# Optimization experiments

Measured on AMD Instinct MI355X. Metric: run time of the kernel, lower is better.

## Reference

```python
import jax, jax.numpy as jnp
import numpy as np

IN_C = 1024
MID = 256
S_C = 256
TOPK_FRAC = 0.25  # atten_topk in (0,1) -> fraction of H*W


def stanh(x):
    return 1.7159 * jnp.tanh(2.0 * x / 3.0)


def setup_inputs() -> dict:
    key = jax.random.key(0)
    ks = jax.random.split(key, 5)
    B, H, W = 32, 28, 28
    x = jax.random.normal(ks[0], (B, IN_C, H, W), jnp.float32)
    s = jax.random.normal(ks[1], (B, S_C), jnp.float32)
    Wq_w = jax.random.normal(ks[2], (MID, IN_C), jnp.float32) * 0.02
    Wq_b = jnp.zeros((MID,), jnp.float32)
    Uq_w = jax.random.normal(ks[3], (MID, S_C), jnp.float32) * 0.02
    w_w = jax.random.normal(ks[4], (IN_C, MID), jnp.float32) * 0.02
    w_b = jnp.zeros((IN_C,), jnp.float32)
    return {"x": x, "s": s, "Wq_w": Wq_w, "Wq_b": Wq_b, "Uq_w": Uq_w, "w_w": w_w, "w_b": w_b}


def reference(x, s, Wq_w, Wq_b, Uq_w, w_w, w_b):
    B, C, H, W = x.shape
    # 1x1 conv Wq(x) + Uq(s) broadcast over spatial, then scaled tanh
    proj = (jnp.einsum('bchw,mc->bmhw', x, Wq_w)
            + Wq_b[None, :, None, None]
            + jnp.einsum('bs,ms->bm', s, Uq_w)[:, :, None, None])
    sig = stanh(proj)  # [B, MID, H, W]
    # 1x1 conv back to in_channel
    alpha = jnp.einsum('bmhw,cm->bchw', sig, w_w) + w_b[None, :, None, None]
    alpha = alpha.reshape(B, C, H * W)
    # topk threshold per (b, c): zero out entries strictly below the k-th largest
    k = int(TOPK_FRAC * H * W)
    th = jax.lax.top_k(alpha, k)[0][..., -1:]  # [B, C, 1]
    alpha = jnp.where(alpha < th, jnp.zeros_like(alpha), alpha)
    # softmax over spatial dim (zeros still contribute exp(0), matching torch)
    atten = jax.nn.softmax(alpha, axis=2)  # [B, C, HW]
    # weighted spatial reduce: c[b,c] = sum_n x[b,c,n] * atten[b,c,n]
    c = jnp.einsum('bcn,bcn->bc', x.reshape(B, C, -1), atten)
    return (c, atten)
```

## Files before the change

### kernel.cpp

```cpp
#include <hip/hip_runtime.h>
#include <hip/hip_bf16.h>
#include <hip/hip_fp16.h>
#include <math.h>

#define BATCH 32
#define INC 1024
#define MIDC 256
#define SC 256
#define HW 784
#define ROWS 25088
#define KSEL 196

typedef _Float16 f16;
typedef __attribute__((ext_vector_type(8))) _Float16 hfrag;
typedef __attribute__((ext_vector_type(4))) float f4;

struct alignas(8) h4s { f16 x, y, z, w; };

__device__ inline float stanh_fast(float p) {
    float e = __expf(1.33333333f * p);
    return 1.7159f * (1.0f - 2.0f / (e + 1.0f));
}

__global__ __launch_bounds__(256) void cvt_f16(const float* __restrict__ src,
                                               f16* __restrict__ dst, int n4) {
    int i = blockIdx.x * 256 + threadIdx.x;
    if (i >= n4) return;
    float4 v = ((const float4*)src)[i];
    h4s h = { (f16)v.x, (f16)v.y, (f16)v.z, (f16)v.w };
    ((h4s*)dst)[i] = h;
}

__global__ __launch_bounds__(256) void prep_x(const float* __restrict__ x,
                                              f16* __restrict__ xh) {
    int b = blockIdx.z, c0 = blockIdx.y * 32, n0 = blockIdx.x * 32;
    __shared__ float tile[32][33];
    int t = threadIdx.x;
    int r = t >> 3, cg = (t & 7) * 4;
    if (n0 + cg + 3 < HW) {
        float4 v = *(const float4*)(x + (size_t)(b * INC + c0 + r) * HW + n0 + cg);
        tile[r][cg + 0] = v.x; tile[r][cg + 1] = v.y;
        tile[r][cg + 2] = v.z; tile[r][cg + 3] = v.w;
    }
    __syncthreads();
    int rn = t >> 3, cg2 = (t & 7) * 4;
    int n = n0 + rn;
    if (n < HW) {
        h4s h = { (f16)tile[cg2 + 0][rn], (f16)tile[cg2 + 1][rn],
                  (f16)tile[cg2 + 2][rn], (f16)tile[cg2 + 3][rn] };
        *(h4s*)(xh + ((size_t)b * HW + n) * INC + c0 + cg2) = h;
    }
}

__global__ __launch_bounds__(256) void calc_u(const float* __restrict__ s,
                                              const float* __restrict__ Uq_w,
                                              const float* __restrict__ Wq_b,
                                              float* __restrict__ u) {
    __shared__ float ssh[SC];
    int b = blockIdx.x, m = threadIdx.x;
    ssh[m] = s[b * SC + m];
    __syncthreads();
    float acc = Wq_b[m];
    const float* uq = Uq_w + (size_t)m * SC;
    #pragma unroll 8
    for (int i = 0; i < SC; ++i) acc += ssh[i] * uq[i];
    u[b * MIDC + m] = acc;
}

__global__ __launch_bounds__(256) void gemm1_mfma(
    const f16* __restrict__ A,
    const f16* __restrict__ B,
    const float* __restrict__ u,
    f16* __restrict__ S) {
    const int R0 = blockIdx.x * 64;
    const int M0 = blockIdx.y * 128;
    __shared__ f16 Asm[128][40];
    __shared__ f16 Bsm[64][40];
    const int t = threadIdx.x;
    const int lane = t & 63, w = t >> 6;
    const int wc = (w >> 1) * 64;
    const int wr = (w & 1) * 32;
    const int ln = lane & 15, kg = lane >> 4;

    const int ar0 = t >> 2, ar1 = ar0 + 64;
    const int akc = (t & 3) * 8;
    const size_t aoff0 = (size_t)(M0 + ar0) * INC + akc;
    const size_t aoff1 = (size_t)(M0 + ar1) * INC + akc;
    const size_t boff  = (size_t)(R0 + ar0) * INC + akc;

    f4 acc[4][2];
    const f4 zero = {0.f, 0.f, 0.f, 0.f};
    #pragma unroll
    for (int i = 0; i < 4; ++i) { acc[i][0] = zero; acc[i][1] = zero; }

    hfrag rA0, rA1, rB;
    #define G1_LOAD(K0)                                   \
        rA0 = *(const hfrag*)(A + aoff0 + (K0));          \
        rA1 = *(const hfrag*)(A + aoff1 + (K0));          \
        rB  = *(const hfrag*)(B + boff  + (K0));

    G1_LOAD(0)
    for (int k0 = 0; k0 < INC; k0 += 32) {
        *(hfrag*)&Asm[ar0][akc] = rA0;
        *(hfrag*)&Asm[ar1][akc] = rA1;
        *(hfrag*)&Bsm[ar0][akc] = rB;
        __syncthreads();
        if (k0 + 32 < INC) { G1_LOAD(k0 + 32) }
        hfrag b0 = *(const hfrag*)&Bsm[wr + ln][kg * 8];
        hfrag b1 = *(const hfrag*)&Bsm[wr + 16 + ln][kg * 8];
        #pragma unroll
        for (int mi = 0; mi < 4; ++mi) {
            hfrag a = *(const hfrag*)&Asm[wc + mi * 16 + ln][kg * 8];
            acc[mi][0] = __builtin_amdgcn_mfma_f32_16x16x32_f16(a, b0, acc[mi][0], 0, 0, 0);
            acc[mi][1] = __builtin_amdgcn_mfma_f32_16x16x32_f16(a, b1, acc[mi][1], 0, 0, 0);
        }
        __syncthreads();
    }
    #undef G1_LOAD

    #pragma unroll
    for (int ni = 0; ni < 2; ++ni) {
        int R = R0 + wr + ni * 16 + ln;
        int b = R / HW;
        #pragma unroll
        for (int mi = 0; mi < 4; ++mi) {
            int mb = M0 + wc + mi * 16 + kg * 4;
            float uv[4];
            *(float4*)uv = *(const float4*)(u + b * MIDC + mb);
            h4s hv;
            hv.x = (f16)stanh_fast(acc[mi][ni][0] + uv[0]);
            hv.y = (f16)stanh_fast(acc[mi][ni][1] + uv[1]);
            hv.z = (f16)stanh_fast(acc[mi][ni][2] + uv[2]);
            hv.w = (f16)stanh_fast(acc[mi][ni][3] + uv[3]);
            *(h4s*)(S + (size_t)R * MIDC + mb) = hv;
        }
    }
}

__global__ __launch_bounds__(256) void gemm2_mfma(
    const f16* __restrict__ A,
    const f16* __restrict__ B,
    const float* __restrict__ wb,
    float* __restrict__ aout) {
    const int R0 = blockIdx.x * 128;
    const int C0 = blockIdx.y * 128;
    __shared__ f16 Asm[128][40];
    __shared__ f16 Bsm[128][40];
    const int t = threadIdx.x;
    const int lane = t & 63, w = t >> 6;
    const int wc = (w >> 1) * 64;
    const int wr = (w & 1) * 64;
    const int ln = lane & 15, kg = lane >> 4;

    const int r0 = t >> 2, r1 = r0 + 64;
    const int kc = (t & 3) * 8;
    const size_t aoff0 = (size_t)(C0 + r0) * MIDC + kc;
    const size_t aoff1 = (size_t)(C0 + r1) * MIDC + kc;
    const size_t boff0 = (size_t)(R0 + r0) * MIDC + kc;
    const size_t boff1 = (size_t)(R0 + r1) * MIDC + kc;

    f4 acc[4][4];
    const f4 zero = {0.f, 0.f, 0.f, 0.f};
    #pragma unroll
    for (int i = 0; i < 4; ++i)
        #pragma unroll
        for (int j = 0; j < 4; ++j) acc[i][j] = zero;

    hfrag rA0, rA1, rB0, rB1;
    #define G2_LOAD(K0)                                   \
        rA0 = *(const hfrag*)(A + aoff0 + (K0));          \
        rA1 = *(const hfrag*)(A + aoff1 + (K0));          \
        rB0 = *(const hfrag*)(B + boff0 + (K0));          \
        rB1 = *(const hfrag*)(B + boff1 + (K0));

    G2_LOAD(0)
    for (int k0 = 0; k0 < MIDC; k0 += 32) {
        *(hfrag*)&Asm[r0][kc] = rA0;
        *(hfrag*)&Asm[r1][kc] = rA1;
        *(hfrag*)&Bsm[r0][kc] = rB0;
        *(hfrag*)&Bsm[r1][kc] = rB1;
        __syncthreads();
        if (k0 + 32 < MIDC) { G2_LOAD(k0 + 32) }
        hfrag bh[4];
        #pragma unroll
        for (int ni = 0; ni < 4; ++ni)
            bh[ni] = *(const hfrag*)&Bsm[wr + ni * 16 + ln][kg * 8];
        #pragma unroll
        for (int mi = 0; mi < 4; ++mi) {
            hfrag a = *(const hfrag*)&Asm[wc + mi * 16 + ln][kg * 8];
            #pragma unroll
            for (int ni = 0; ni < 4; ++ni)
                acc[mi][ni] = __builtin_amdgcn_mfma_f32_16x16x32_f16(a, bh[ni], acc[mi][ni], 0, 0, 0);
        }
        __syncthreads();
    }
    #undef G2_LOAD

    #pragma unroll
    for (int ni = 0; ni < 4; ++ni) {
        int R = R0 + wr + ni * 16 + ln;
        int b = R / HW;
        int n = R - b * HW;
        float* arow = aout + (size_t)b * INC * HW + n;
        #pragma unroll
        for (int mi = 0; mi < 4; ++mi) {
            int cb = C0 + wc + mi * 16 + kg * 4;
            float wv[4];
            *(float4*)wv = *(const float4*)(wb + cb);
            #pragma unroll
            for (int r = 0; r < 4; ++r)
                arow[(size_t)(cb + r) * HW] = acc[mi][ni][r] + wv[r];
        }
    }
}

__global__ __launch_bounds__(256) void topk_softmax_reduce(const float* __restrict__ x,
                                                           float* __restrict__ out) {
    const int wid  = threadIdx.x >> 6;
    const int lane = threadIdx.x & 63;
    const int row  = blockIdx.x * 4 + wid;
    float* arow = out + BATCH * INC + (size_t)row * HW;
    const float* xrow = x + (size_t)row * HW;

    __shared__ int hist[4][4][264];
    int* hp0 = &hist[wid][0][0];
    const int g = lane >> 4;

    const bool has3 = (lane < 4);
    float4 v4[4];
    uint32_t key[16];

    {
        const float4* ap = (const float4*)arow;
        v4[0] = ap[lane];
        v4[1] = ap[lane + 64];
        v4[2] = ap[lane + 128];
        v4[3] = has3 ? ap[192 + lane] : make_float4(0.f, 0.f, 0.f, 0.f);
    }
    const float* vv = (const float*)v4;
    #pragma unroll
    for (int i = 0; i < 16; ++i) {
        bool ok = (i < 12) | has3;
        uint32_t uu = __float_as_uint(vv[i]);
        uint32_t k = (uu & 0x80000000u) ? ~uu : (uu | 0x80000000u);
        key[i] = ok ? k : 0u;
    }

    int kk = KSEL;
    uint32_t prefix = 0;
    uint32_t thkey = 0;
    bool done = false;

    #pragma unroll
    for (int round = 0; round < 4; ++round) {
        if (!done) {
            const int shift = 24 - 8 * round;
            const int4 z4 = {0, 0, 0, 0};
            if (round == 0) {
                #pragma unroll
                for (int j = 0; j < 5; ++j) {
                    int idx = lane + 64 * j;
                    if (idx < 264) ((int4*)hp0)[idx] = z4;
                }
                #pragma unroll
                for (int i = 0; i < 16; ++i)
                    if (key[i]) atomicAdd(&hist[wid][g][key[i] >> 24], 1);
            } else {
                ((int4*)hp0)[lane] = z4;
                const uint32_t himask = 0xFFFFFFFFu << (shift + 8);
                #pragma unroll
                for (int i = 0; i < 16; ++i)
                    if ((key[i] & himask) == prefix)
                        atomicAdd(&hp0[(key[i] >> shift) & 255], 1);
            }

            int h0, h1, h2, h3;
            if (round == 0) {
                int4 c0 = *(const int4*)&hist[wid][0][4 * lane];
                int4 c1 = *(const int4*)&hist[wid][1][4 * lane];
                int4 c2 = *(const int4*)&hist[wid][2][4 * lane];
                int4 c3 = *(const int4*)&hist[wid][3][4 * lane];
                h0 = c0.x + c1.x + c2.x + c3.x;
                h1 = c0.y + c1.y + c2.y + c3.y;
                h2 = c0.z + c1.z + c2.z + c3.z;
                h3 = c0.w + c1.w + c2.w + c3.w;
            } else {
                int4 c = *(const int4*)&hp0[4 * lane];
                h0 = c.x; h1 = c.y; h2 = c.z; h3 = c.w;
            }
            int gsum = h0 + h1 + h2 + h3;
            int suf = gsum;
            #pragma unroll
            for (int off = 1; off < 64; off <<= 1) {
                int o = __shfl_down(suf, off, 64);
                suf += (lane + off < 64) ? o : 0;
            }
            int ex = suf - gsum;
            int cgt3 = ex, cgt2 = cgt3 + h3, cgt1 = cgt2 + h2, cgt0 = cgt1 + h1;
            int bsel = -1, cg = 0, hs = 0;
            if (cgt0 < kk && kk <= cgt0 + h0) { bsel = 4 * lane + 0; cg = cgt0; hs = h0; }
            if (cgt1 < kk && kk <= cgt1 + h1) { bsel = 4 * lane + 1; cg = cgt1; hs = h1; }
            if (cgt2 < kk && kk <= cgt2 + h2) { bsel = 4 * lane + 2; cg = cgt2; hs = h2; }
            if (cgt3 < kk && kk <= cgt3 + h3) { bsel = 4 * lane + 3; cg = cgt3; hs = h3; }
            unsigned long long m = __ballot(bsel >= 0);
            int src = (int)__ffsll((long long)m) - 1;
            bsel = __shfl(bsel, src, 64);
            cg   = __shfl(cg,   src, 64);
            hs   = __shfl(hs,   src, 64);
            kk -= cg;
            prefix |= ((uint32_t)bsel) << shift;

            if (shift == 0) {
                thkey = prefix;
                done = true;
            } else if (kk == 1 || kk == hs) {
                const uint32_t maskP = 0xFFFFFFFFu << shift;
                bool want_max = (kk == 1);
                uint32_t r = want_max ? 0u : 0xFFFFFFFFu;
                #pragma unroll
                for (int i = 0; i < 16; ++i) {
                    if ((key[i] & maskP) == prefix)
                        r = want_max ? (r > key[i] ? r : key[i])
                                     : (r < key[i] ? r : key[i]);
                }
                #pragma unroll
                for (int off = 32; off; off >>= 1) {
                    uint32_t o = __shfl_xor(r, off, 64);
                    r = want_max ? (r > o ? r : o) : (r < o ? r : o);
                }
                thkey = r;
                done = true;
            }
        }
    }

    uint32_t tu = (thkey & 0x80000000u) ? (thkey ^ 0x80000000u) : ~thkey;
    const float th = __uint_as_float(tu);

    float* vw = (float*)v4;
    float mx = -INFINITY;
    #pragma unroll
    for (int i = 0; i < 16; ++i) {
        bool ok = (i < 12) | has3;
        float f = vw[i];
        f = (f < th) ? 0.0f : f;
        vw[i] = f;
        if (ok) mx = fmaxf(mx, f);
    }
    #pragma unroll
    for (int off = 32; off; off >>= 1) mx = fmaxf(mx, __shfl_xor(mx, off, 64));

    float sum = 0.f;
    #pragma unroll
    for (int i = 0; i < 16; ++i) {
        bool ok = (i < 12) | has3;
        float e = __expf(vw[i] - mx);
        vw[i] = e;
        sum += ok ? e : 0.f;
    }
    #pragma unroll
    for (int off = 32; off; off >>= 1) sum += __shfl_xor(sum, off, 64);
    float inv = 1.0f / sum;

    float dot = 0.f;
    {
        float4* ap = (float4*)arow;
        const float4* xp = (const float4*)xrow;
        #pragma unroll
        for (int ci = 0; ci < 4; ++ci) {
            if (ci == 3 && !has3) break;
            int chunk = (ci < 3) ? (lane + 64 * ci) : (192 + lane);
            float4 a;
            a.x = vw[ci * 4 + 0] * inv;
            a.y = vw[ci * 4 + 1] * inv;
            a.z = vw[ci * 4 + 2] * inv;
            a.w = vw[ci * 4 + 3] * inv;
            ap[chunk] = a;
            float4 xl = xp[chunk];
            dot += xl.x * a.x + xl.y * a.y + xl.z * a.z + xl.w * a.w;
        }
    }
    #pragma unroll
    for (int off = 32; off; off >>= 1) dot += __shfl_xor(dot, off, 64);
    if (lane == 0) out[row] = dot;
}

extern "C" void kernel_launch(void* const* d_in, const int* in_sizes, int n_in,
                              void* d_out, int out_size, void* d_ws, size_t ws_size,
                              hipStream_t stream) {
    const float* x    = (const float*)d_in[0];
    const float* s    = (const float*)d_in[1];
    const float* Wq_w = (const float*)d_in[2];
    const float* Wq_b = (const float*)d_in[3];
    const float* Uq_w = (const float*)d_in[4];
    const float* w_w  = (const float*)d_in[5];
    const float* w_b  = (const float*)d_in[6];
    float* out = (float*)d_out;

    f16* xt   = (f16*)d_ws;
    f16* sig  = xt + (size_t)ROWS * INC;
    f16* wq_h = sig + (size_t)ROWS * MIDC;
    f16* ww_h = wq_h + MIDC * INC;
    float* u  = (float*)(ww_h + INC * MIDC);
    float* alpha = out + BATCH * INC;

    cvt_f16<<<256, 256, 0, stream>>>(Wq_w, wq_h, MIDC * INC / 4);
    cvt_f16<<<256, 256, 0, stream>>>(w_w, ww_h, INC * MIDC / 4);
    prep_x<<<dim3(25, 32, 32), 256, 0, stream>>>(x, xt);
    calc_u<<<BATCH, 256, 0, stream>>>(s, Uq_w, Wq_b, u);
    gemm1_mfma<<<dim3(ROWS / 64, 2), 256, 0, stream>>>(wq_h, xt, u, sig);
    gemm2_mfma<<<dim3(ROWS / 128, 8), 256, 0, stream>>>(ww_h, sig, w_b, alpha);
    topk_softmax_reduce<<<BATCH * INC / 4, 256, 0, stream>>>(x, out);
}
```

Baseline: 179.4 us.

## Replace 8-bit radix top-k select with adaptive min/max range-binned selection

Replaces the fixed 256-bin radix select over key bytes with an iterative selection that bins the current candidates into 64 buckets scaled linearly between their wave-wide min and max. The narrowing bucket is tracked as a per-lane candidate bitmask. Adaptive range binning should isolate the k-th value in fewer rounds with a smaller shared histogram and a single-element-per-lane scan instead of four. The trade-offs are extra min/max shuffle reductions and a float multiply per key each iteration. The loop has no fixed number of iterations, and float rounding in the bin computation needs care.

```diff
diff --git a/kernel.cpp b/kernel.cpp
--- a/kernel.cpp
+++ b/kernel.cpp
@@ -222,7 +222,7 @@
     float* arow = out + BATCH * INC + (size_t)row * HW;
     const float* xrow = x + (size_t)row * HW;
 
-    __shared__ int hist[4][4][264];
+    __shared__ int hist[4][4][72];
     int* hp0 = &hist[wid][0][0];
     const int g = lane >> 4;
 
@@ -240,98 +240,91 @@
     const float* vv = (const float*)v4;
     #pragma unroll
     for (int i = 0; i < 16; ++i) {
-        bool ok = (i < 12) | has3;
         uint32_t uu = __float_as_uint(vv[i]);
-        uint32_t k = (uu & 0x80000000u) ? ~uu : (uu | 0x80000000u);
-        key[i] = ok ? k : 0u;
-    }
-
+        key[i] = (uu & 0x80000000u) ? ~uu : (uu | 0x80000000u);
+    }
+
+    uint32_t cand = has3 ? 0xFFFFu : 0x0FFFu;
     int kk = KSEL;
-    uint32_t prefix = 0;
     uint32_t thkey = 0;
-    bool done = false;
-
-    #pragma unroll
-    for (int round = 0; round < 4; ++round) {
-        if (!done) {
-            const int shift = 24 - 8 * round;
-            const int4 z4 = {0, 0, 0, 0};
-            if (round == 0) {
-                #pragma unroll
-                for (int j = 0; j < 5; ++j) {
-                    int idx = lane + 64 * j;
-                    if (idx < 264) ((int4*)hp0)[idx] = z4;
-                }
-                #pragma unroll
-                for (int i = 0; i < 16; ++i)
-                    if (key[i]) atomicAdd(&hist[wid][g][key[i] >> 24], 1);
-            } else {
-                ((int4*)hp0)[lane] = z4;
-                const uint32_t himask = 0xFFFFFFFFu << (shift + 8);
-                #pragma unroll
-                for (int i = 0; i < 16; ++i)
-                    if ((key[i] & himask) == prefix)
-                        atomicAdd(&hp0[(key[i] >> shift) & 255], 1);
+
+    for (int iter = 0; iter < 16; ++iter) {
+        uint32_t umin = 0xFFFFFFFFu, umax = 0u;
+        #pragma unroll
+        for (int i = 0; i < 16; ++i) {
+            if ((cand >> i) & 1) {
+                uint32_t kc = key[i];
+                umin = umin < kc ? umin : kc;
+                umax = umax > kc ? umax : kc;
             }
-
-            int h0, h1, h2, h3;
-            if (round == 0) {
-                int4 c0 = *(const int4*)&hist[wid][0][4 * lane];
-                int4 c1 = *(const int4*)&hist[wid][1][4 * lane];
-                int4 c2 = *(const int4*)&hist[wid][2][4 * lane];
-                int4 c3 = *(const int4*)&hist[wid][3][4 * lane];
-                h0 = c0.x + c1.x + c2.x + c3.x;
-                h1 = c0.y + c1.y + c2.y + c3.y;
-                h2 = c0.z + c1.z + c2.z + c3.z;
-                h3 = c0.w + c1.w + c2.w + c3.w;
-            } else {
-                int4 c = *(const int4*)&hp0[4 * lane];
-                h0 = c.x; h1 = c.y; h2 = c.z; h3 = c.w;
+        }
+        #pragma unroll
+        for (int off = 32; off; off >>= 1) {
+            uint32_t omn = (uint32_t)__shfl_xor((int)umin, off, 64);
+            uint32_t omx = (uint32_t)__shfl_xor((int)umax, off, 64);
+            umin = umin < omn ? umin : omn;
+            umax = umax > omx ? umax : omx;
+        }
+        thkey = umin;
+        if (umin == umax) break;
+        const float scale = 63.999f / (float)(umax - umin);
+
+        const int4 z4 = {0, 0, 0, 0};
+        ((int4*)hp0)[lane] = z4;
+        if (lane < 8) ((int4*)hp0)[64 + lane] = z4;
+        #pragma unroll
+        for (int i = 0; i < 16; ++i) {
+            if ((cand >> i) & 1) {
+                int bn = (int)((float)(key[i] - umin) * scale);
+                atomicAdd(&hist[wid][g][bn], 1);
             }
-            int gsum = h0 + h1 + h2 + h3;
-            int suf = gsum;
+        }
+
+        int h = hist[wid][0][lane] + hist[wid][1][lane]
+              + hist[wid][2][lane] + hist[wid][3][lane];
+        int suf = h;
+        #pragma unroll
+        for (int off = 1; off < 64; off <<= 1) {
+            int o = __shfl_down(suf, off, 64);
+            suf += (lane + off < 64) ? o : 0;
+        }
+        int cgt = suf - h;
+        bool hit = (cgt < kk && kk <= cgt + h);
+        unsigned long long m = __ballot(hit);
+        int bsel = (int)__ffsll((long long)m) - 1;
+        int cg = __shfl(cgt, bsel, 64);
+        int hs = __shfl(h,   bsel, 64);
+        kk -= cg;
+
+        bool exit_max = (kk == 1), exit_min = (kk == hs);
+        if (exit_max | exit_min) {
+            uint32_t r = exit_max ? 0u : 0xFFFFFFFFu;
             #pragma unroll
-            for (int off = 1; off < 64; off <<= 1) {
-                int o = __shfl_down(suf, off, 64);
-                suf += (lane + off < 64) ? o : 0;
-            }
-            int ex = suf - gsum;
-            int cgt3 = ex, cgt2 = cgt3 + h3, cgt1 = cgt2 + h2, cgt0 = cgt1 + h1;
-            int bsel = -1, cg = 0, hs = 0;
-            if (cgt0 < kk && kk <= cgt0 + h0) { bsel = 4 * lane + 0; cg = cgt0; hs = h0; }
-            if (cgt1 < kk && kk <= cgt1 + h1) { bsel = 4 * lane + 1; cg = cgt1; hs = h1; }
-            if (cgt2 < kk && kk <= cgt2 + h2) { bsel = 4 * lane + 2; cg = cgt2; hs = h2; }
-            if (cgt3 < kk && kk <= cgt3 + h3) { bsel = 4 * lane + 3; cg = cgt3; hs = h3; }
-            unsigned long long m = __ballot(bsel >= 0);
-            int src = (int)__ffsll((long long)m) - 1;
-            bsel = __shfl(bsel, src, 64);
-            cg   = __shfl(cg,   src, 64);
-            hs   = __shfl(hs,   src, 64);
-            kk -= cg;
-            prefix |= ((uint32_t)bsel) << shift;
-
-            if (shift == 0) {
-                thkey = prefix;
-                done = true;
-            } else if (kk == 1 || kk == hs) {
-                const uint32_t maskP = 0xFFFFFFFFu << shift;
-                bool want_max = (kk == 1);
-                uint32_t r = want_max ? 0u : 0xFFFFFFFFu;
-                #pragma unroll
-                for (int i = 0; i < 16; ++i) {
-                    if ((key[i] & maskP) == prefix)
-                        r = want_max ? (r > key[i] ? r : key[i])
+            for (int i = 0; i < 16; ++i) {
+                if ((cand >> i) & 1) {
+                    int bn = (int)((float)(key[i] - umin) * scale);
+                    if (bn == bsel)
+                        r = exit_max ? (r > key[i] ? r : key[i])
                                      : (r < key[i] ? r : key[i]);
                 }
-                #pragma unroll
-                for (int off = 32; off; off >>= 1) {
-                    uint32_t o = __shfl_xor(r, off, 64);
-                    r = want_max ? (r > o ? r : o) : (r < o ? r : o);
-                }
-                thkey = r;
-                done = true;
             }
-        }
+            #pragma unroll
+            for (int off = 32; off; off >>= 1) {
+                uint32_t o = (uint32_t)__shfl_xor((int)r, off, 64);
+                r = exit_max ? (r > o ? r : o) : (r < o ? r : o);
+            }
+            thkey = r;
+            break;
+        }
+        uint32_t nc = 0;
+        #pragma unroll
+        for (int i = 0; i < 16; ++i) {
+            if ((cand >> i) & 1) {
+                int bn = (int)((float)(key[i] - umin) * scale);
+                if (bn == bsel) nc |= (1u << i);
+            }
+        }
+        cand = nc;
     }
 
     uint32_t tu = (thkey & 0x80000000u) ? (thkey ^ 0x80000000u) : ~thkey;
```

After: 198.9 us. 10.9% more time.

## Fuse x transpose and f16 conversion into first GEMM with full-M tiles

Applied to the files above, without the earlier changes.

Removes the separate prep_x kernel, which transposed x into an f16 row-major workspace. gemm1 now loads fp32 x tiles straight from NCHW, transposes and converts them through shared memory, and computes all 256 mid channels per block over 112-row tiles (7x4 MFMA tiles per wave). This saves a full write and re-read of the transposed activation. In exchange it adds an extra shared-memory pass and barrier per k-step, raises register pressure from 28 accumulators, and launches fewer blocks (224).

```diff
diff --git a/kernel.cpp b/kernel.cpp
--- a/kernel.cpp
+++ b/kernel.cpp
@@ -10,6 +10,7 @@
 #define HW 784
 #define ROWS 25088
 #define KSEL 196
+#define BM1 112
 
 typedef _Float16 f16;
 typedef __attribute__((ext_vector_type(8))) _Float16 hfrag;
@@ -29,27 +30,6 @@
     float4 v = ((const float4*)src)[i];
     h4s h = { (f16)v.x, (f16)v.y, (f16)v.z, (f16)v.w };
     ((h4s*)dst)[i] = h;
-}
-
-__global__ __launch_bounds__(256) void prep_x(const float* __restrict__ x,
-                                              f16* __restrict__ xh) {
-    int b = blockIdx.z, c0 = blockIdx.y * 32, n0 = blockIdx.x * 32;
-    __shared__ float tile[32][33];
-    int t = threadIdx.x;
-    int r = t >> 3, cg = (t & 7) * 4;
-    if (n0 + cg + 3 < HW) {
-        float4 v = *(const float4*)(x + (size_t)(b * INC + c0 + r) * HW + n0 + cg);
-        tile[r][cg + 0] = v.x; tile[r][cg + 1] = v.y;
-        tile[r][cg + 2] = v.z; tile[r][cg + 3] = v.w;
-    }
-    __syncthreads();
-    int rn = t >> 3, cg2 = (t & 7) * 4;
-    int n = n0 + rn;
-    if (n < HW) {
-        h4s h = { (f16)tile[cg2 + 0][rn], (f16)tile[cg2 + 1][rn],
-                  (f16)tile[cg2 + 2][rn], (f16)tile[cg2 + 3][rn] };
-        *(h4s*)(xh + ((size_t)b * HW + n) * INC + c0 + cg2) = h;
-    }
 }
 
 __global__ __launch_bounds__(256) void calc_u(const float* __restrict__ s,
@@ -67,71 +47,107 @@
     u[b * MIDC + m] = acc;
 }
 
-__global__ __launch_bounds__(256) void gemm1_mfma(
-    const f16* __restrict__ A,
-    const f16* __restrict__ B,
+__global__ __launch_bounds__(256) void gemm1_fused(
+    const float* __restrict__ x,
+    const f16* __restrict__ Wq,
     const float* __restrict__ u,
     f16* __restrict__ S) {
-    const int R0 = blockIdx.x * 64;
-    const int M0 = blockIdx.y * 128;
-    __shared__ f16 Asm[128][40];
-    __shared__ f16 Bsm[64][40];
+    const int R0 = blockIdx.x * BM1;
+    const int b  = R0 / HW;
+    const int n0 = R0 - b * HW;
+    __shared__ f16   Asm[256][40];
+    __shared__ float Xf[32][116];
+    __shared__ f16   Bsm[BM1][40];
+
     const int t = threadIdx.x;
     const int lane = t & 63, w = t >> 6;
-    const int wc = (w >> 1) * 64;
-    const int wr = (w & 1) * 32;
+    const int wc = w * 64;
     const int ln = lane & 15, kg = lane >> 4;
 
-    const int ar0 = t >> 2, ar1 = ar0 + 64;
-    const int akc = (t & 3) * 8;
-    const size_t aoff0 = (size_t)(M0 + ar0) * INC + akc;
-    const size_t aoff1 = (size_t)(M0 + ar1) * INC + akc;
-    const size_t boff  = (size_t)(R0 + ar0) * INC + akc;
-
-    f4 acc[4][2];
+    const int arow = t >> 2;
+
+    const float* xb = x + ((size_t)b * INC) * HW + n0;
+
+    f4 acc[7][4];
     const f4 zero = {0.f, 0.f, 0.f, 0.f};
     #pragma unroll
-    for (int i = 0; i < 4; ++i) { acc[i][0] = zero; acc[i][1] = zero; }
-
-    hfrag rA0, rA1, rB;
-    #define G1_LOAD(K0)                                   \
-        rA0 = *(const hfrag*)(A + aoff0 + (K0));          \
-        rA1 = *(const hfrag*)(A + aoff1 + (K0));          \
-        rB  = *(const hfrag*)(B + boff  + (K0));
-
-    G1_LOAD(0)
+    for (int i = 0; i < 7; ++i)
+        #pragma unroll
+        for (int j = 0; j < 4; ++j) acc[i][j] = zero;
+
+    float4 rx[4];
+    hfrag  rA[4];
+
+    #define LOAD_TILES(K0)                                                     \
+        _Pragma("unroll")                                                      \
+        for (int it = 0; it < 4; ++it) {                                       \
+            int cid = t + it * 256;                                            \
+            rA[it] = *(const hfrag*)(Wq + (size_t)(cid >> 2) * INC + (K0) + (cid & 3) * 8); \
+        }                                                                      \
+        _Pragma("unroll")                                                      \
+        for (int it = 0; it < 4; ++it) {                                       \
+            int fid = t + it * 256;                                            \
+            if (fid < 896) {                                                   \
+                int cr = fid / 28, nc = (fid % 28) * 4;                        \
+                rx[it] = *(const float4*)(xb + (size_t)((K0) + cr) * HW + nc); \
+            }                                                                  \
+        }
+
+    LOAD_TILES(0)
     for (int k0 = 0; k0 < INC; k0 += 32) {
-        *(hfrag*)&Asm[ar0][akc] = rA0;
-        *(hfrag*)&Asm[ar1][akc] = rA1;
-        *(hfrag*)&Bsm[ar0][akc] = rB;
+        #pragma unroll
+        for (int it = 0; it < 4; ++it) {
+            int cid = t + it * 256;
+            *(hfrag*)&Asm[cid >> 2][(cid & 3) * 8] = rA[it];
+        }
+        #pragma unroll
+        for (int it = 0; it < 4; ++it) {
+            int fid = t + it * 256;
+            if (fid < 896)
+                *(float4*)&Xf[fid / 28][(fid % 28) * 4] = rx[it];
+        }
         __syncthreads();
-        if (k0 + 32 < INC) { G1_LOAD(k0 + 32) }
-        hfrag b0 = *(const hfrag*)&Bsm[wr + ln][kg * 8];
-        hfrag b1 = *(const hfrag*)&Bsm[wr + 16 + ln][kg * 8];
+        #pragma unroll
+        for (int it = 0; it < 4; ++it) {
+            int q = t + it * 256;
+            if (q < 896) {
+                int n = q % 112, cq = (q / 112) * 4;
+                h4s hv = { (f16)Xf[cq + 0][n], (f16)Xf[cq + 1][n],
+                           (f16)Xf[cq + 2][n], (f16)Xf[cq + 3][n] };
+                *(h4s*)&Bsm[n][cq] = hv;
+            }
+        }
+        if (k0 + 32 < INC) { LOAD_TILES(k0 + 32) }
+        __syncthreads();
+        hfrag bf[7];
+        #pragma unroll
+        for (int ri = 0; ri < 7; ++ri)
+            bf[ri] = *(const hfrag*)&Bsm[ri * 16 + ln][kg * 8];
         #pragma unroll
         for (int mi = 0; mi < 4; ++mi) {
             hfrag a = *(const hfrag*)&Asm[wc + mi * 16 + ln][kg * 8];
-            acc[mi][0] = __builtin_amdgcn_mfma_f32_16x16x32_f16(a, b0, acc[mi][0], 0, 0, 0);
-            acc[mi][1] = __builtin_amdgcn_mfma_f32_16x16x32_f16(a, b1, acc[mi][1], 0, 0, 0);
+            #pragma unroll
+            for (int ri = 0; ri < 7; ++ri)
+                acc[ri][mi] = __builtin_amdgcn_mfma_f32_16x16x32_f16(a, bf[ri], acc[ri][mi], 0, 0, 0);
         }
         __syncthreads();
     }
-    #undef G1_LOAD
-
-    #pragma unroll
-    for (int ni = 0; ni < 2; ++ni) {
-        int R = R0 + wr + ni * 16 + ln;
-        int b = R / HW;
+    #undef LOAD_TILES
+
+    const float* ub = u + b * MIDC;
+    #pragma unroll
+    for (int ri = 0; ri < 7; ++ri) {
+        int R = R0 + ri * 16 + ln;
         #pragma unroll
         for (int mi = 0; mi < 4; ++mi) {
-            int mb = M0 + wc + mi * 16 + kg * 4;
+            int mb = wc + mi * 16 + kg * 4;
             float uv[4];
-            *(float4*)uv = *(const float4*)(u + b * MIDC + mb);
+            *(float4*)uv = *(const float4*)(ub + mb);
             h4s hv;
-            hv.x = (f16)stanh_fast(acc[mi][ni][0] + uv[0]);
-            hv.y = (f16)stanh_fast(acc[mi][ni][1] + uv[1]);
-            hv.z = (f16)stanh_fast(acc[mi][ni][2] + uv[2]);
-            hv.w = (f16)stanh_fast(acc[mi][ni][3] + uv[3]);
+            hv.x = (f16)stanh_fast(acc[ri][mi][0] + uv[0]);
+            hv.y = (f16)stanh_fast(acc[ri][mi][1] + uv[1]);
+            hv.z = (f16)stanh_fast(acc[ri][mi][2] + uv[2]);
+            hv.w = (f16)stanh_fast(acc[ri][mi][3] + uv[3]);
             *(h4s*)(S + (size_t)R * MIDC + mb) = hv;
         }
     }
@@ -397,8 +413,7 @@
     const float* w_b  = (const float*)d_in[6];
     float* out = (float*)d_out;
 
-    f16* xt   = (f16*)d_ws;
-    f16* sig  = xt + (size_t)ROWS * INC;
+    f16* sig  = (f16*)d_ws;
     f16* wq_h = sig + (size_t)ROWS * MIDC;
     f16* ww_h = wq_h + MIDC * INC;
     float* u  = (float*)(ww_h + INC * MIDC);
@@ -406,9 +421,8 @@
 
     cvt_f16<<<256, 256, 0, stream>>>(Wq_w, wq_h, MIDC * INC / 4);
     cvt_f16<<<256, 256, 0, stream>>>(w_w, ww_h, INC * MIDC / 4);
-    prep_x<<<dim3(25, 32, 32), 256, 0, stream>>>(x, xt);
     calc_u<<<BATCH, 256, 0, stream>>>(s, Uq_w, Wq_b, u);
-    gemm1_mfma<<<dim3(ROWS / 64, 2), 256, 0, stream>>>(wq_h, xt, u, sig);
+    gemm1_fused<<<ROWS / BM1, 256, 0, stream>>>(x, wq_h, u, sig);
     gemm2_mfma<<<dim3(ROWS / 128, 8), 256, 0, stream>>>(ww_h, sig, w_b, alpha);
     topk_softmax_reduce<<<BATCH * INC / 4, 256, 0, stream>>>(x, out);
 }
```

New measurement: 205.5 us. 1.15x slower.

## Fuse second GEMM with top-k softmax reduce via shared-memory alpha tile

Applied to the files above, without the earlier changes.

Merges the second projection GEMM and the top-k/softmax/reduce kernel into one kernel. Each block computes a 16-channel by 784-position alpha tile for one batch into LDS with MFMA, then each wave runs the radix-select threshold, softmax and weighted reduce straight from shared memory. This removes the global write and re-read of the full fp32 alpha tensor that sat between the two kernels. In exchange, the GEMM no longer reuses tiles (each block re-reads the sig rows for its batch, and A fragments are held in registers), and the large LDS footprint lowers occupancy.

```diff
diff --git a/kernel.cpp b/kernel.cpp
--- a/kernel.cpp
+++ b/kernel.cpp
@@ -137,252 +137,209 @@
     }
 }
 
-__global__ __launch_bounds__(256) void gemm2_mfma(
+__global__ __launch_bounds__(256) void gemm2_topk(
     const f16* __restrict__ A,
     const f16* __restrict__ B,
     const float* __restrict__ wb,
-    float* __restrict__ aout) {
-    const int R0 = blockIdx.x * 128;
-    const int C0 = blockIdx.y * 128;
-    __shared__ f16 Asm[128][40];
-    __shared__ f16 Bsm[128][40];
+    const float* __restrict__ x,
+    float* __restrict__ out) {
+    const int b  = blockIdx.y;
+    const int c0 = blockIdx.x * 16;
     const int t = threadIdx.x;
     const int lane = t & 63, w = t >> 6;
-    const int wc = (w >> 1) * 64;
-    const int wr = (w & 1) * 64;
     const int ln = lane & 15, kg = lane >> 4;
 
-    const int r0 = t >> 2, r1 = r0 + 64;
-    const int kc = (t & 3) * 8;
-    const size_t aoff0 = (size_t)(C0 + r0) * MIDC + kc;
-    const size_t aoff1 = (size_t)(C0 + r1) * MIDC + kc;
-    const size_t boff0 = (size_t)(R0 + r0) * MIDC + kc;
-    const size_t boff1 = (size_t)(R0 + r1) * MIDC + kc;
-
-    f4 acc[4][4];
-    const f4 zero = {0.f, 0.f, 0.f, 0.f};
+    __shared__ float alpha[16][788];
+    __shared__ int hist[4][2][264];
+
+    hfrag a[8];
     #pragma unroll
-    for (int i = 0; i < 4; ++i)
-        #pragma unroll
-        for (int j = 0; j < 4; ++j) acc[i][j] = zero;
-
-    hfrag rA0, rA1, rB0, rB1;
-    #define G2_LOAD(K0)                                   \
-        rA0 = *(const hfrag*)(A + aoff0 + (K0));          \
-        rA1 = *(const hfrag*)(A + aoff1 + (K0));          \
-        rB0 = *(const hfrag*)(B + boff0 + (K0));          \
-        rB1 = *(const hfrag*)(B + boff1 + (K0));
-
-    G2_LOAD(0)
-    for (int k0 = 0; k0 < MIDC; k0 += 32) {
-        *(hfrag*)&Asm[r0][kc] = rA0;
-        *(hfrag*)&Asm[r1][kc] = rA1;
-        *(hfrag*)&Bsm[r0][kc] = rB0;
-        *(hfrag*)&Bsm[r1][kc] = rB1;
-        __syncthreads();
-        if (k0 + 32 < MIDC) { G2_LOAD(k0 + 32) }
-        hfrag bh[4];
-        #pragma unroll
-        for (int ni = 0; ni < 4; ++ni)
-            bh[ni] = *(const hfrag*)&Bsm[wr + ni * 16 + ln][kg * 8];
-        #pragma unroll
-        for (int mi = 0; mi < 4; ++mi) {
-            hfrag a = *(const hfrag*)&Asm[wc + mi * 16 + ln][kg * 8];
+    for (int k0 = 0; k0 < 8; ++k0)
+        a[k0] = *(const hfrag*)(A + (size_t)(c0 + ln) * MIDC + k0 * 32 + kg * 8);
+    float4 wv = *(const float4*)(wb + c0 + kg * 4);
+
+    const int tstart = (w == 0) ? 0 : (13 + (w - 1) * 12);
+    const int tcnt   = (w == 0) ? 13 : 12;
+    const size_t Rbase = (size_t)b * HW;
+
+    for (int ti = 0; ti < tcnt; ++ti) {
+        const int nt = tstart + ti;
+        const size_t boff = (Rbase + nt * 16 + ln) * MIDC + kg * 8;
+        hfrag bb[8];
+        #pragma unroll
+        for (int k0 = 0; k0 < 8; ++k0)
+            bb[k0] = *(const hfrag*)(B + boff + k0 * 32);
+        f4 ac = {0.f, 0.f, 0.f, 0.f};
+        #pragma unroll
+        for (int k0 = 0; k0 < 8; ++k0)
+            ac = __builtin_amdgcn_mfma_f32_16x16x32_f16(a[k0], bb[k0], ac, 0, 0, 0);
+        #pragma unroll
+        for (int r = 0; r < 4; ++r)
+            alpha[4 * kg + r][nt * 16 + ln] = ac[r] + ((const float*)&wv)[r];
+    }
+    __syncthreads();
+
+    int* hp0 = &hist[w][0][0];
+    const int g = lane >> 5;
+    const bool has3 = (lane < 4);
+
+    for (int rr = 0; rr < 4; ++rr) {
+        const int cl  = w + rr * 4;
+        const int row = b * INC + c0 + cl;
+        float* arow = out + BATCH * INC + (size_t)row * HW;
+        const float* xrow = x + (size_t)row * HW;
+        const float4* lp = (const float4*)&alpha[cl][0];
+
+        float4 v4[4];
+        v4[0] = lp[lane];
+        v4[1] = lp[lane + 64];
+        v4[2] = lp[lane + 128];
+        v4[3] = has3 ? lp[192 + lane] : make_float4(0.f, 0.f, 0.f, 0.f);
+
+        const float* vv = (const float*)v4;
+        uint32_t key[16];
+        #pragma unroll
+        for (int i = 0; i < 16; ++i) {
+            bool ok = (i < 12) | has3;
+            uint32_t uu = __float_as_uint(vv[i]);
+            uint32_t k = (uu & 0x80000000u) ? ~uu : (uu | 0x80000000u);
+            key[i] = ok ? k : 0u;
+        }
+
+        int kk = KSEL;
+        uint32_t prefix = 0;
+        uint32_t thkey = 0;
+        bool done = false;
+
+        #pragma unroll
+        for (int round = 0; round < 4; ++round) {
+            if (!done) {
+                const int shift = 24 - 8 * round;
+                const int4 z4 = {0, 0, 0, 0};
+                if (round == 0) {
+                    #pragma unroll
+                    for (int j = 0; j < 3; ++j) {
+                        int idx = lane + 64 * j;
+                        if (idx < 132) ((int4*)hp0)[idx] = z4;
+                    }
+                    #pragma unroll
+                    for (int i = 0; i < 16; ++i)
+                        if (key[i]) atomicAdd(&hist[w][g][key[i] >> 24], 1);
+                } else {
+                    ((int4*)hp0)[lane] = z4;
+                    const uint32_t himask = 0xFFFFFFFFu << (shift + 8);
+                    #pragma unroll
+                    for (int i = 0; i < 16; ++i)
+                        if ((key[i] & himask) == prefix)
+                            atomicAdd(&hp0[(key[i] >> shift) & 255], 1);
+                }
+
+                int h0, h1, h2, h3;
+                if (round == 0) {
+                    int4 ca = *(const int4*)&hist[w][0][4 * lane];
+                    int4 cb = *(const int4*)&hist[w][1][4 * lane];
+                    h0 = ca.x + cb.x; h1 = ca.y + cb.y;
+                    h2 = ca.z + cb.z; h3 = ca.w + cb.w;
+                } else {
+                    int4 c = *(const int4*)&hp0[4 * lane];
+                    h0 = c.x; h1 = c.y; h2 = c.z; h3 = c.w;
+                }
+                int gsum = h0 + h1 + h2 + h3;
+                int suf = gsum;
+                #pragma unroll
+                for (int off = 1; off < 64; off <<= 1) {
+                    int o = __shfl_down(suf, off, 64);
+                    suf += (lane + off < 64) ? o : 0;
+                }
+                int ex = suf - gsum;
+                int cgt3 = ex, cgt2 = cgt3 + h3, cgt1 = cgt2 + h2, cgt0 = cgt1 + h1;
+                int bsel = -1, cg = 0, hs = 0;
+                if (cgt0 < kk && kk <= cgt0 + h0) { bsel = 4 * lane + 0; cg = cgt0; hs = h0; }
+                if (cgt1 < kk && kk <= cgt1 + h1) { bsel = 4 * lane + 1; cg = cgt1; hs = h1; }
+                if (cgt2 < kk && kk <= cgt2 + h2) { bsel = 4 * lane + 2; cg = cgt2; hs = h2; }
+                if (cgt3 < kk && kk <= cgt3 + h3) { bsel = 4 * lane + 3; cg = cgt3; hs = h3; }
+                unsigned long long m = __ballot(bsel >= 0);
+                int src = (int)__ffsll((long long)m) - 1;
+                bsel = __shfl(bsel, src, 64);
+                cg   = __shfl(cg,   src, 64);
+                hs   = __shfl(hs,   src, 64);
+                kk -= cg;
+                prefix |= ((uint32_t)bsel) << shift;
+
+                if (shift == 0) {
+                    thkey = prefix;
+                    done = true;
+                } else if (kk == 1 || kk == hs) {
+                    const uint32_t maskP = 0xFFFFFFFFu << shift;
+                    bool want_max = (kk == 1);
+                    uint32_t r = want_max ? 0u : 0xFFFFFFFFu;
+                    #pragma unroll
+                    for (int i = 0; i < 16; ++i) {
+                        if ((key[i] & maskP) == prefix)
+                            r = want_max ? (r > key[i] ? r : key[i])
+                                         : (r < key[i] ? r : key[i]);
+                    }
+                    #pragma unroll
+                    for (int off = 32; off; off >>= 1) {
+                        uint32_t o = __shfl_xor(r, off, 64);
+                        r = want_max ? (r > o ? r : o) : (r < o ? r : o);
+                    }
+                    thkey = r;
+                    done = true;
+                }
+            }
+        }
+
+        uint32_t tu = (thkey & 0x80000000u) ? (thkey ^ 0x80000000u) : ~thkey;
+        const float th = __uint_as_float(tu);
+
+        float* vwp = (float*)v4;
+        float mx = -INFINITY;
+        #pragma unroll
+        for (int i = 0; i < 16; ++i) {
+            bool ok = (i < 12) | has3;
+            float f = vwp[i];
+            f = (f < th) ? 0.0f : f;
+            vwp[i] = f;
+            if (ok) mx = fmaxf(mx, f);
+        }
+        #pragma unroll
+        for (int off = 32; off; off >>= 1) mx = fmaxf(mx, __shfl_xor(mx, off, 64));
+
+        float sum = 0.f;
+        #pragma unroll
+        for (int i = 0; i < 16; ++i) {
+            bool ok = (i < 12) | has3;
+            float e = __expf(vwp[i] - mx);
+            vwp[i] = e;
+            sum += ok ? e : 0.f;
+        }
+        #pragma unroll
+        for (int off = 32; off; off >>= 1) sum += __shfl_xor(sum, off, 64);
+        float inv = 1.0f / sum;
+
+        float dot = 0.f;
+        {
+            float4* ap = (float4*)arow;
+            const float4* xp = (const float4*)xrow;
             #pragma unroll
-            for (int ni = 0; ni < 4; ++ni)
-                acc[mi][ni] = __builtin_amdgcn_mfma_f32_16x16x32_f16(a, bh[ni], acc[mi][ni], 0, 0, 0);
-        }
-        __syncthreads();
-    }
-    #undef G2_LOAD
-
-    #pragma unroll
-    for (int ni = 0; ni < 4; ++ni) {
-        int R = R0 + wr + ni * 16 + ln;
-        int b = R / HW;
-        int n = R - b * HW;
-        float* arow = aout + (size_t)b * INC * HW + n;
-        #pragma unroll
-        for (int mi = 0; mi < 4; ++mi) {
-            int cb = C0 + wc + mi * 16 + kg * 4;
-            float wv[4];
-            *(float4*)wv = *(const float4*)(wb + cb);
-            #pragma unroll
-            for (int r = 0; r < 4; ++r)
-                arow[(size_t)(cb + r) * HW] = acc[mi][ni][r] + wv[r];
-        }
-    }
-}
-
-__global__ __launch_bounds__(256) void topk_softmax_reduce(const float* __restrict__ x,
-                                                           float* __restrict__ out) {
-    const int wid  = threadIdx.x >> 6;
-    const int lane = threadIdx.x & 63;
-    const int row  = blockIdx.x * 4 + wid;
-    float* arow = out + BATCH * INC + (size_t)row * HW;
-    const float* xrow = x + (size_t)row * HW;
-
-    __shared__ int hist[4][4][264];
-    int* hp0 = &hist[wid][0][0];
-    const int g = lane >> 4;
-
-    const bool has3 = (lane < 4);
-    float4 v4[4];
-    uint32_t key[16];
-
-    {
-        const float4* ap = (const float4*)arow;
-        v4[0] = ap[lane];
-        v4[1] = ap[lane + 64];
-        v4[2] = ap[lane + 128];
-        v4[3] = has3 ? ap[192 + lane] : make_float4(0.f, 0.f, 0.f, 0.f);
-    }
-    const float* vv = (const float*)v4;
-    #pragma unroll
-    for (int i = 0; i < 16; ++i) {
-        bool ok = (i < 12) | has3;
-        uint32_t uu = __float_as_uint(vv[i]);
-        uint32_t k = (uu & 0x80000000u) ? ~uu : (uu | 0x80000000u);
-        key[i] = ok ? k : 0u;
-    }
-
-    int kk = KSEL;
-    uint32_t prefix = 0;
-    uint32_t thkey = 0;
-    bool done = false;
-
-    #pragma unroll
-    for (int round = 0; round < 4; ++round) {
-        if (!done) {
-            const int shift = 24 - 8 * round;
-            const int4 z4 = {0, 0, 0, 0};
-            if (round == 0) {
-                #pragma unroll
-                for (int j = 0; j < 5; ++j) {
-                    int idx = lane + 64 * j;
-                    if (idx < 264) ((int4*)hp0)[idx] = z4;
-                }
-                #pragma unroll
-                for (int i = 0; i < 16; ++i)
-                    if (key[i]) atomicAdd(&hist[wid][g][key[i] >> 24], 1);
-            } else {
-                ((int4*)hp0)[lane] = z4;
-                const uint32_t himask = 0xFFFFFFFFu << (shift + 8);
-                #pragma unroll
-                for (int i = 0; i < 16; ++i)
-                    if ((key[i] & himask) == prefix)
-                        atomicAdd(&hp0[(key[i] >> shift) & 255], 1);
+            for (int ci = 0; ci < 4; ++ci) {
+                if (ci == 3 && !has3) break;
+                int chunk = (ci < 3) ? (lane + 64 * ci) : (192 + lane);
+                float4 av;
+                av.x = vwp[ci * 4 + 0] * inv;
+                av.y = vwp[ci * 4 + 1] * inv;
+                av.z = vwp[ci * 4 + 2] * inv;
+                av.w = vwp[ci * 4 + 3] * inv;
+                ap[chunk] = av;
+                float4 xl = xp[chunk];
+                dot += xl.x * av.x + xl.y * av.y + xl.z * av.z + xl.w * av.w;
             }
-
-            int h0, h1, h2, h3;
-            if (round == 0) {
-                int4 c0 = *(const int4*)&hist[wid][0][4 * lane];
-                int4 c1 = *(const int4*)&hist[wid][1][4 * lane];
-                int4 c2 = *(const int4*)&hist[wid][2][4 * lane];
-                int4 c3 = *(const int4*)&hist[wid][3][4 * lane];
-                h0 = c0.x + c1.x + c2.x + c3.x;
-                h1 = c0.y + c1.y + c2.y + c3.y;
-                h2 = c0.z + c1.z + c2.z + c3.z;
-                h3 = c0.w + c1.w + c2.w + c3.w;
-            } else {
-                int4 c = *(const int4*)&hp0[4 * lane];
-                h0 = c.x; h1 = c.y; h2 = c.z; h3 = c.w;
-            }
-            int gsum = h0 + h1 + h2 + h3;
-            int suf = gsum;
-            #pragma unroll
-            for (int off = 1; off < 64; off <<= 1) {
-                int o = __shfl_down(suf, off, 64);
-                suf += (lane + off < 64) ? o : 0;
-            }
-            int ex = suf - gsum;
-            int cgt3 = ex, cgt2 = cgt3 + h3, cgt1 = cgt2 + h2, cgt0 = cgt1 + h1;
-            int bsel = -1, cg = 0, hs = 0;
-            if (cgt0 < kk && kk <= cgt0 + h0) { bsel = 4 * lane + 0; cg = cgt0; hs = h0; }
-            if (cgt1 < kk && kk <= cgt1 + h1) { bsel = 4 * lane + 1; cg = cgt1; hs = h1; }
-            if (cgt2 < kk && kk <= cgt2 + h2) { bsel = 4 * lane + 2; cg = cgt2; hs = h2; }
-            if (cgt3 < kk && kk <= cgt3 + h3) { bsel = 4 * lane + 3; cg = cgt3; hs = h3; }
-            unsigned long long m = __ballot(bsel >= 0);
-            int src = (int)__ffsll((long long)m) - 1;
-            bsel = __shfl(bsel, src, 64);
-            cg   = __shfl(cg,   src, 64);
-            hs   = __shfl(hs,   src, 64);
-            kk -= cg;
-            prefix |= ((uint32_t)bsel) << shift;
-
-            if (shift == 0) {
-                thkey = prefix;
-                done = true;
-            } else if (kk == 1 || kk == hs) {
-                const uint32_t maskP = 0xFFFFFFFFu << shift;
-                bool want_max = (kk == 1);
-                uint32_t r = want_max ? 0u : 0xFFFFFFFFu;
-                #pragma unroll
-                for (int i = 0; i < 16; ++i) {
-                    if ((key[i] & maskP) == prefix)
-                        r = want_max ? (r > key[i] ? r : key[i])
-                                     : (r < key[i] ? r : key[i]);
-                }
-                #pragma unroll
-                for (int off = 32; off; off >>= 1) {
-                    uint32_t o = __shfl_xor(r, off, 64);
-                    r = want_max ? (r > o ? r : o) : (r < o ? r : o);
-                }
-                thkey = r;
-                done = true;
-            }
-        }
-    }
-
-    uint32_t tu = (thkey & 0x80000000u) ? (thkey ^ 0x80000000u) : ~thkey;
-    const float th = __uint_as_float(tu);
-
-    float* vw = (float*)v4;
-    float mx = -INFINITY;
-    #pragma unroll
-    for (int i = 0; i < 16; ++i) {
-        bool ok = (i < 12) | has3;
-        float f = vw[i];
-        f = (f < th) ? 0.0f : f;
-        vw[i] = f;
-        if (ok) mx = fmaxf(mx, f);
-    }
-    #pragma unroll
-    for (int off = 32; off; off >>= 1) mx = fmaxf(mx, __shfl_xor(mx, off, 64));
-
-    float sum = 0.f;
-    #pragma unroll
-    for (int i = 0; i < 16; ++i) {
-        bool ok = (i < 12) | has3;
-        float e = __expf(vw[i] - mx);
-        vw[i] = e;
-        sum += ok ? e : 0.f;
-    }
-    #pragma unroll
-    for (int off = 32; off; off >>= 1) sum += __shfl_xor(sum, off, 64);
-    float inv = 1.0f / sum;
-
-    float dot = 0.f;
-    {
-        float4* ap = (float4*)arow;
-        const float4* xp = (const float4*)xrow;
-        #pragma unroll
-        for (int ci = 0; ci < 4; ++ci) {
-            if (ci == 3 && !has3) break;
-            int chunk = (ci < 3) ? (lane + 64 * ci) : (192 + lane);
-            float4 a;
-            a.x = vw[ci * 4 + 0] * inv;
-            a.y = vw[ci * 4 + 1] * inv;
-            a.z = vw[ci * 4 + 2] * inv;
-            a.w = vw[ci * 4 + 3] * inv;
-            ap[chunk] = a;
-            float4 xl = xp[chunk];
-            dot += xl.x * a.x + xl.y * a.y + xl.z * a.z + xl.w * a.w;
-        }
-    }
-    #pragma unroll
-    for (int off = 32; off; off >>= 1) dot += __shfl_xor(dot, off, 64);
-    if (lane == 0) out[row] = dot;
+        }
+        #pragma unroll
+        for (int off = 32; off; off >>= 1) dot += __shfl_xor(dot, off, 64);
+        if (lane == 0) out[row] = dot;
+    }
 }
 
 extern "C" void kernel_launch(void* const* d_in, const int* in_sizes, int n_in,
@@ -402,13 +359,11 @@
     f16* wq_h = sig + (size_t)ROWS * MIDC;
     f16* ww_h = wq_h + MIDC * INC;
     float* u  = (float*)(ww_h + INC * MIDC);
-    float* alpha = out + BATCH * INC;
 
     cvt_f16<<<256, 256, 0, stream>>>(Wq_w, wq_h, MIDC * INC / 4);
     cvt_f16<<<256, 256, 0, stream>>>(w_w, ww_h, INC * MIDC / 4);
+    calc_u<<<BATCH, 256, 0, stream>>>(s, Uq_w, Wq_b, u);
     prep_x<<<dim3(25, 32, 32), 256, 0, stream>>>(x, xt);
-    calc_u<<<BATCH, 256, 0, stream>>>(s, Uq_w, Wq_b, u);
     gemm1_mfma<<<dim3(ROWS / 64, 2), 256, 0, stream>>>(wq_h, xt, u, sig);
-    gemm2_mfma<<<dim3(ROWS / 128, 8), 256, 0, stream>>>(ww_h, sig, w_b, alpha);
-    topk_softmax_reduce<<<BATCH * INC / 4, 256, 0, stream>>>(x, out);
-}
+    gemm2_topk<<<dim3(INC / 16, BATCH), 256, 0, stream>>>(ww_h, sig, w_b, x, out);
+}
```

Result: slower. 261.0 us (+45.5%).
